# Performance work log

Hardware: AMD Instinct MI355X
Metric: run time of the kernel (lower is better)

## Reference

```python
import jax, jax.numpy as jnp
import numpy as np

IN_FEATURES = 1024
OUT_FEATURES = 1024
GRID_SIZE = 8
SPLINE_ORDER = 3
NUM_CTRL = GRID_SIZE + SPLINE_ORDER  # 11


def _make_grid():
    h = 2.0 / GRID_SIZE
    return jnp.linspace(-1.0 - SPLINE_ORDER * h, 1.0 + SPLINE_ORDER * h,
                        GRID_SIZE + 2 * SPLINE_ORDER + 1, dtype=jnp.float32)  # [15]


def b_splines(t, grid, order):
    # t: [B, F] (already tanh'd). Vectorized over all features at once —
    # the torch per-feature Python loop computes identical math per column.
    te = t[..., None]  # [B, F, 1]
    basis = ((te >= grid[:-1]) & (te < grid[1:])).astype(t.dtype)  # [B, F, G-1]
    for k in range(1, order + 1):
        left_den = grid[k:-1] - grid[:-k - 1]
        left_den = jnp.where(left_den == 0, jnp.ones_like(left_den), left_den)
        left = (te - grid[:-k - 1]) / left_den * basis[..., :-1]
        right_den = grid[k + 1:] - grid[1:-k]
        right_den = jnp.where(right_den == 0, jnp.ones_like(right_den), right_den)
        right = (grid[k + 1:] - te) / right_den * basis[..., 1:]
        basis = left + right
    return basis  # [B, F, NUM_CTRL]


def setup_inputs() -> dict:
    key = jax.random.key(0)
    kx, kc, kw = jax.random.split(key, 3)
    x = jax.random.normal(kx, (4096, IN_FEATURES), dtype=jnp.float32)
    coeffs = jax.random.normal(kc, (IN_FEATURES, OUT_FEATURES, NUM_CTRL), dtype=jnp.float32) * 0.05
    base_weight = jax.random.normal(kw, (IN_FEATURES, OUT_FEATURES), dtype=jnp.float32) * 0.05
    grid = _make_grid()
    return {"x": x, "coeffs": coeffs, "base_weight": base_weight, "grid": grid}


def reference(x, coeffs, base_weight, grid):
    bases = b_splines(jnp.tanh(x), grid, SPLINE_ORDER)          # [B, in, n]
    activation = jnp.einsum('bin,ion->bo', bases, coeffs)        # [B, out]
    residual = x @ base_weight                                   # [B, out]
    return activation + residual
```

## Files before the change

kernel.cpp:

```cpp
#include <hip/hip_runtime.h>
#include <hip/hip_bf16.h>

typedef __attribute__((ext_vector_type(8))) short bf16x8;
typedef __attribute__((ext_vector_type(4))) float f32x4;
typedef __attribute__((ext_vector_type(8))) unsigned short u16x8;

#define M_DIM 4096
#define N_DIM 1024
#define IN_F  1024
#define K_DIM 12288
#define KS4   4
#define KPART (K_DIM / KS4)
#define BK 64
#define NT (KPART / BK)

__device__ __forceinline__ unsigned short f2b(float v) {
  __hip_bfloat16 h = __float2bfloat16(v);
  return *reinterpret_cast<unsigned short*>(&h);
}

__device__ __forceinline__ float fast_tanh(float x) {
  float e = __expf(2.0f * x);
  return 1.0f - 2.0f / (e + 1.0f);
}

__device__ __forceinline__ void spline12(float xv, float* w) {
  float t  = fast_tanh(xv);
  float tf = (t + 1.75f) * 4.0f;
  int j = (int)tf;
  j = j < 3 ? 3 : (j > 10 ? 10 : j);
  float u  = tf - (float)j;
  float um = 1.0f - u;
  float u2 = u * u;
  float w0 = um * um * um * (1.0f / 6.0f);
  float w1 = (0.5f * u - 1.0f) * u2 + (2.0f / 3.0f);
  float w2 = ((-0.5f * u + 0.5f) * u + 0.5f) * u + (1.0f / 6.0f);
  float w3 = u * u2 * (1.0f / 6.0f);
  int base = j - 3;
  #pragma unroll
  for (int s = 0; s < 11; ++s) {
    int r = s - base;
    w[s] = (r == 0) ? w0 : (r == 1) ? w1 : (r == 2) ? w2 : (r == 3) ? w3 : 0.0f;
  }
  w[11] = xv;
}

__global__ __launch_bounds__(256) void bases_kernel(const float* __restrict__ x,
                                                    unsigned short* __restrict__ A) {
  __shared__ unsigned short sb[256 * 24];
  const int tid = threadIdx.x;
  int e0 = blockIdx.x * 512 + tid * 2;
  float2 xv = *(const float2*)(x + e0);
  float w0[12], w1[12];
  spline12(xv.x, w0);
  spline12(xv.y, w1);
  #pragma unroll
  for (int s = 0; s < 12; ++s) { sb[tid * 24 + s] = f2b(w0[s]); sb[tid * 24 + 12 + s] = f2b(w1[s]); }
  __syncthreads();
  u16x8* dst = (u16x8*)(A + (size_t)blockIdx.x * 512 * 12);
  const u16x8* src = (const u16x8*)sb;
  #pragma unroll
  for (int k = 0; k < 3; ++k) dst[tid + k * 256] = src[tid + k * 256];
}

__global__ __launch_bounds__(256) void repack_kernel(const float* __restrict__ coeffs,
                                                     const float* __restrict__ W,
                                                     unsigned short* __restrict__ Bt) {
  __shared__ float lc[64 * 180];
  __shared__ float lw[64 * 20];
  const int o0 = blockIdx.x * 16;
  const int i0 = blockIdx.y * 64;
  const int tid = threadIdx.x;
  #pragma unroll
  for (int it = 0; it < 11; ++it) {
    int v = it * 256 + tid;
    int i = v / 44, c = v - i * 44;
    f32x4 d = *(const f32x4*)(coeffs + ((size_t)(i0 + i) * 1024 + o0) * 11 + c * 4);
    *(f32x4*)(lc + i * 180 + c * 4) = d;
  }
  #pragma unroll
  for (int it = 0; it < 4; ++it) {
    int e = it * 256 + tid;
    int i = e >> 4, ol = e & 15;
    lw[i * 20 + ol] = W[(size_t)(i0 + i) * 1024 + o0 + ol];
  }
  __syncthreads();
  #pragma unroll
  for (int it = 0; it < 6; ++it) {
    int v = it * 256 + tid;
    int ol = v / 96, c = v - ol * 96;
    unsigned short h[8];
    #pragma unroll
    for (int s = 0; s < 8; ++s) {
      int g = c * 8 + s;
      int i = g / 12, n = g - i * 12;
      float val = (n < 11) ? lc[i * 180 + ol * 11 + n] : lw[i * 20 + ol];
      h[s] = f2b(val);
    }
    *(u16x8*)(Bt + (size_t)(o0 + ol) * K_DIM + (size_t)i0 * 12 + c * 8) =
        (u16x8){h[0], h[1], h[2], h[3], h[4], h[5], h[6], h[7]};
  }
}

__device__ __forceinline__ void async16(const void* g, void* l) {
  __builtin_amdgcn_global_load_lds(
      (const __attribute__((address_space(1))) void*)g,
      (__attribute__((address_space(3))) void*)l, 16, 0, 0);
}

__global__ __launch_bounds__(512, 2) void gemm_kernel(const unsigned short* __restrict__ A,
                                                      const unsigned short* __restrict__ Bt,
                                                      float* __restrict__ out) {
  __shared__ __align__(16) unsigned short lds[65536];
  char* lp = (char*)lds;
  const int AS[2] = {0, 32768};
  const int BS[2] = {65536, 98304};

  const int tid  = threadIdx.x;
  const int lane = tid & 63;
  const int wid  = tid >> 6;
  const int wm   = wid >> 2;
  const int wn   = wid & 3;

  const int blk = blockIdx.x;
  const int xcd = blk & 7;
  const int q   = blk >> 3;
  const int bm  = xcd * 2 + (q & 1);
  const int r2  = q >> 1;
  const int bn  = r2 & 3;
  const int ks  = r2 >> 2;
  const size_t m0 = (size_t)bm * 256;
  const size_t n0 = (size_t)bn * 256;
  const size_t ksbyte = (size_t)ks * KPART * 2;

  const char* srcA[4]; const char* srcB[4]; int ldso[4];
  #pragma unroll
  for (int p = 0; p < 4; ++p) {
    int g  = p * 512 + tid;
    int rr = g >> 3, cp = g & 7;
    int cs = cp ^ (rr & 7);
    srcA[p] = (const char*)A  + ((m0 + rr) * (size_t)K_DIM) * 2 + ksbyte + cs * 16;
    srcB[p] = (const char*)Bt + ((n0 + rr) * (size_t)K_DIM) * 2 + ksbyte + cs * 16;
    ldso[p] = g * 16;
  }

  auto stage = [&](int slot, int tile) {
    size_t kb = (size_t)tile * 128;
    #pragma unroll
    for (int p = 0; p < 4; ++p) async16(srcA[p] + kb, lp + AS[slot] + ldso[p]);
    #pragma unroll
    for (int p = 0; p < 4; ++p) async16(srcB[p] + kb, lp + BS[slot] + ldso[p]);
  };

  int offA[8], offB[4];
  #pragma unroll
  for (int m = 0; m < 8; ++m) {
    int row = wm * 128 + m * 16 + (lane & 15);
    int ck  = (lane >> 4) ^ (row & 7);
    offA[m] = row * 128 + ck * 16;
  }
  #pragma unroll
  for (int n = 0; n < 4; ++n) {
    int rowb = wn * 64 + n * 16 + (lane & 15);
    int ckb  = (lane >> 4) ^ (rowb & 7);
    offB[n] = rowb * 128 + ckb * 16;
  }

  f32x4 acc[8][4];
  #pragma unroll
  for (int m = 0; m < 8; ++m)
    #pragma unroll
    for (int n = 0; n < 4; ++n) acc[m][n] = (f32x4){0.f, 0.f, 0.f, 0.f};

  stage(0, 0);
  stage(1, 1);

  for (int t = 0; t < NT; ++t) {
    const int cur = t & 1;
    if (t < NT - 1) asm volatile("s_waitcnt vmcnt(8)" ::: "memory");
    else            asm volatile("s_waitcnt vmcnt(0)" ::: "memory");
    __builtin_amdgcn_s_barrier();
    __builtin_amdgcn_sched_barrier(0);
    asm volatile("" ::: "memory");

    __builtin_amdgcn_s_setprio(1);
    #pragma unroll
    for (int kk = 0; kk < 2; ++kk) {
      const int kx = kk * 64;
      bf16x8 a[8], b[4];
      #pragma unroll
      for (int m = 0; m < 8; ++m) a[m] = *(const bf16x8*)(lp + AS[cur] + (offA[m] ^ kx));
      #pragma unroll
      for (int n = 0; n < 4; ++n) b[n] = *(const bf16x8*)(lp + BS[cur] + (offB[n] ^ kx));
      #pragma unroll
      for (int m = 0; m < 8; ++m)
        #pragma unroll
        for (int n = 0; n < 4; ++n)
          acc[m][n] = __builtin_amdgcn_mfma_f32_16x16x32_bf16(a[m], b[n], acc[m][n], 0, 0, 0);
    }
    __builtin_amdgcn_s_setprio(0);

    asm volatile("" ::: "memory");
    __builtin_amdgcn_sched_barrier(0);
    __builtin_amdgcn_s_barrier();

    if (t + 2 < NT) stage(cur, t + 2);
  }

  const int lr = (lane >> 4) * 4;
  const int lc = lane & 15;
  #pragma unroll
  for (int m = 0; m < 8; ++m)
    #pragma unroll
    for (int n = 0; n < 4; ++n)
      #pragma unroll
      for (int j = 0; j < 4; ++j)
        atomicAdd(&out[(m0 + wm * 128 + m * 16 + lr + j) * N_DIM + n0 + wn * 64 + n * 16 + lc],
                  acc[m][n][j]);
}

__global__ __launch_bounds__(256) void fallback_kernel(const float* __restrict__ x,
                                                       const float* __restrict__ coeffs,
                                                       const float* __restrict__ W,
                                                       float* __restrict__ out) {
  __shared__ float bas[16][64][12];
  const int o0 = blockIdx.x * 64;
  const int b0 = blockIdx.y * 16;
  const int tid = threadIdx.x;
  const int o = tid & 63, bg = tid >> 6;
  float acc[4] = {0.f, 0.f, 0.f, 0.f};
  for (int ic = 0; ic < 16; ++ic) {
    __syncthreads();
    #pragma unroll
    for (int p = 0; p < 4; ++p) {
      int pp = tid + p * 256;
      int bb = pp >> 6, il = pp & 63;
      float w[12];
      spline12(x[(size_t)(b0 + bb) * 1024 + ic * 64 + il], w);
      #pragma unroll
      for (int n = 0; n < 12; ++n) bas[bb][il][n] = w[n];
    }
    __syncthreads();
    for (int il = 0; il < 64; ++il) {
      int gi = ic * 64 + il;
      const float* cp = coeffs + ((size_t)gi * 1024 + o0 + o) * 11;
      float cf[12];
      #pragma unroll
      for (int n = 0; n < 11; ++n) cf[n] = cp[n];
      cf[11] = W[(size_t)gi * 1024 + o0 + o];
      #pragma unroll
      for (int bb = 0; bb < 4; ++bb) {
        float s = 0.f;
        #pragma unroll
        for (int n = 0; n < 12; ++n) s += bas[bg * 4 + bb][il][n] * cf[n];
        acc[bb] += s;
      }
    }
  }
  #pragma unroll
  for (int bb = 0; bb < 4; ++bb)
    out[(size_t)(b0 + bg * 4 + bb) * 1024 + o0 + o] = acc[bb];
}

extern "C" void kernel_launch(void* const* d_in, const int* in_sizes, int n_in,
                              void* d_out, int out_size, void* d_ws, size_t ws_size,
                              hipStream_t stream) {
  const float* x      = (const float*)d_in[0];
  const float* coeffs = (const float*)d_in[1];
  const float* W      = (const float*)d_in[2];
  float* out = (float*)d_out;

  const size_t needA = (size_t)M_DIM * K_DIM * 2;
  const size_t needB = (size_t)N_DIM * K_DIM * 2;

  if (ws_size >= needA + needB) {
    unsigned short* Abuf = (unsigned short*)d_ws;
    unsigned short* Btuf = (unsigned short*)((char*)d_ws + needA);
    hipMemsetAsync(out, 0, (size_t)out_size * sizeof(float), stream);
    bases_kernel<<<dim3(M_DIM * IN_F / 512), dim3(256), 0, stream>>>(x, Abuf);
    repack_kernel<<<dim3(64, 16), dim3(256), 0, stream>>>(coeffs, W, Btuf);
    gemm_kernel<<<dim3(256), dim3(512), 0, stream>>>(Abuf, Btuf, out);
  } else {
    fallback_kernel<<<dim3(16, 256), dim3(256), 0, stream>>>(x, coeffs, W, out);
  }
}
```

Baseline: 263.8 us.

## Retile GEMM to 256x128 blocks with triple-buffered 32-wide K chunks

The GEMM tile changes from 256x256 with 512 threads to 256x128 with 256 threads (4 waves, each still 128x64), so the grid grows from 256 to 512 blocks. The K step shrinks from 64 to 32 per stage and uses a three-slot LDS ring, with a paired-row swizzled layout so a 64-byte row chunk fills one 128-byte LDS line. This cuts LDS per block to about 72KB and deepens prefetch, aiming for better occupancy and latency hiding. The cost is more barriers per unit of K, and reuse drops because B tiles are narrower, so A is fetched twice as often.

```diff
diff --git a/kernel.cpp b/kernel.cpp
--- a/kernel.cpp
+++ b/kernel.cpp
@@ -11,8 +11,7 @@
 #define K_DIM 12288
 #define KS4   4
 #define KPART (K_DIM / KS4)
-#define BK 64
-#define NT (KPART / BK)
+#define NC    (KPART / 32)
 
 __device__ __forceinline__ unsigned short f2b(float v) {
   __hip_bfloat16 h = __float2bfloat16(v);
@@ -108,62 +107,73 @@
       (__attribute__((address_space(3))) void*)l, 16, 0, 0);
 }
 
-__global__ __launch_bounds__(512, 2) void gemm_kernel(const unsigned short* __restrict__ A,
+#define REG_SZ 24576
+#define B_OFF  16384
+
+__global__ __launch_bounds__(256, 2) void gemm_kernel(const unsigned short* __restrict__ A,
                                                       const unsigned short* __restrict__ Bt,
                                                       float* __restrict__ out) {
-  __shared__ __align__(16) unsigned short lds[65536];
+  __shared__ __align__(16) unsigned short lds[36864];
   char* lp = (char*)lds;
-  const int AS[2] = {0, 32768};
-  const int BS[2] = {65536, 98304};
 
   const int tid  = threadIdx.x;
   const int lane = tid & 63;
   const int wid  = tid >> 6;
-  const int wm   = wid >> 2;
-  const int wn   = wid & 3;
+  const int wm   = wid >> 1, wn = wid & 1;
 
   const int blk = blockIdx.x;
   const int xcd = blk & 7;
-  const int q   = blk >> 3;
-  const int bm  = xcd * 2 + (q & 1);
-  const int r2  = q >> 1;
-  const int bn  = r2 & 3;
-  const int ks  = r2 >> 2;
+  const int idx = blk >> 3;
+  const int bm  = xcd * 2 + (idx & 1);
+  const int rst = idx >> 1;
+  const int bn  = rst & 7;
+  const int ks  = rst >> 3;
   const size_t m0 = (size_t)bm * 256;
-  const size_t n0 = (size_t)bn * 256;
+  const size_t n0 = (size_t)bn * 128;
   const size_t ksbyte = (size_t)ks * KPART * 2;
 
-  const char* srcA[4]; const char* srcB[4]; int ldso[4];
-  #pragma unroll
-  for (int p = 0; p < 4; ++p) {
-    int g  = p * 512 + tid;
-    int rr = g >> 3, cp = g & 7;
-    int cs = cp ^ (rr & 7);
-    srcA[p] = (const char*)A  + ((m0 + rr) * (size_t)K_DIM) * 2 + ksbyte + cs * 16;
-    srcB[p] = (const char*)Bt + ((n0 + rr) * (size_t)K_DIM) * 2 + ksbyte + cs * 16;
-    ldso[p] = g * 16;
-  }
-
-  auto stage = [&](int slot, int tile) {
-    size_t kb = (size_t)tile * 128;
-    #pragma unroll
-    for (int p = 0; p < 4; ++p) async16(srcA[p] + kb, lp + AS[slot] + ldso[p]);
-    #pragma unroll
-    for (int p = 0; p < 4; ++p) async16(srcB[p] + kb, lp + BS[slot] + ldso[p]);
+  const char* src[6]; int ldst[6];
+  #pragma unroll
+  for (int q = 0; q < 6; ++q) {
+    if (q < 4) {
+      int g  = q * 256 + tid;
+      int rp = g >> 3, cp = g & 7;
+      int c  = cp ^ (rp & 7);
+      int row = (rp << 1) | (c >> 2);
+      src[q]  = (const char*)A + ((m0 + row) * (size_t)K_DIM) * 2 + ksbyte + (c & 3) * 16;
+      ldst[q] = g * 16;
+    } else {
+      int g  = (q - 4) * 256 + tid;
+      int rp = g >> 3, cp = g & 7;
+      int c  = cp ^ (rp & 7);
+      int row = (rp << 1) | (c >> 2);
+      src[q]  = (const char*)Bt + ((n0 + row) * (size_t)K_DIM) * 2 + ksbyte + (c & 3) * 16;
+      ldst[q] = B_OFF + g * 16;
+    }
+  }
+
+  auto stage = [&](int reg, int chunk) {
+    size_t kb = (size_t)chunk * 64;
+    char* rb = lp + reg * REG_SZ;
+    #pragma unroll
+    for (int q = 0; q < 6; ++q) async16(src[q] + kb, rb + ldst[q]);
   };
 
+  const int c2 = lane >> 4;
   int offA[8], offB[4];
   #pragma unroll
   for (int m = 0; m < 8; ++m) {
-    int row = wm * 128 + m * 16 + (lane & 15);
-    int ck  = (lane >> 4) ^ (row & 7);
-    offA[m] = row * 128 + ck * 16;
+    int r  = wm * 128 + m * 16 + (lane & 15);
+    int rp = r >> 1;
+    int cp = (((r & 1) << 2) | c2) ^ (rp & 7);
+    offA[m] = rp * 128 + cp * 16;
   }
   #pragma unroll
   for (int n = 0; n < 4; ++n) {
-    int rowb = wn * 64 + n * 16 + (lane & 15);
-    int ckb  = (lane >> 4) ^ (rowb & 7);
-    offB[n] = rowb * 128 + ckb * 16;
+    int r  = wn * 64 + n * 16 + (lane & 15);
+    int rp = r >> 1;
+    int cp = (((r & 1) << 2) | c2) ^ (rp & 7);
+    offB[n] = B_OFF + rp * 128 + cp * 16;
   }
 
   f32x4 acc[8][4];
@@ -174,24 +184,25 @@
 
   stage(0, 0);
   stage(1, 1);
-
-  for (int t = 0; t < NT; ++t) {
-    const int cur = t & 1;
-    if (t < NT - 1) asm volatile("s_waitcnt vmcnt(8)" ::: "memory");
-    else            asm volatile("s_waitcnt vmcnt(0)" ::: "memory");
+  stage(2, 2);
+
+  int reg = 0;
+  for (int c = 0; c < NC; ++c) {
+    if (c < NC - 2)       asm volatile("s_waitcnt vmcnt(12)" ::: "memory");
+    else if (c == NC - 2) asm volatile("s_waitcnt vmcnt(6)"  ::: "memory");
+    else                  asm volatile("s_waitcnt vmcnt(0)"  ::: "memory");
     __builtin_amdgcn_s_barrier();
     __builtin_amdgcn_sched_barrier(0);
     asm volatile("" ::: "memory");
 
+    char* rb = lp + reg * REG_SZ;
     __builtin_amdgcn_s_setprio(1);
-    #pragma unroll
-    for (int kk = 0; kk < 2; ++kk) {
-      const int kx = kk * 64;
+    {
       bf16x8 a[8], b[4];
       #pragma unroll
-      for (int m = 0; m < 8; ++m) a[m] = *(const bf16x8*)(lp + AS[cur] + (offA[m] ^ kx));
-      #pragma unroll
-      for (int n = 0; n < 4; ++n) b[n] = *(const bf16x8*)(lp + BS[cur] + (offB[n] ^ kx));
+      for (int m = 0; m < 8; ++m) a[m] = *(const bf16x8*)(rb + offA[m]);
+      #pragma unroll
+      for (int n = 0; n < 4; ++n) b[n] = *(const bf16x8*)(rb + offB[n]);
       #pragma unroll
       for (int m = 0; m < 8; ++m)
         #pragma unroll
@@ -204,7 +215,8 @@
     __builtin_amdgcn_sched_barrier(0);
     __builtin_amdgcn_s_barrier();
 
-    if (t + 2 < NT) stage(cur, t + 2);
+    if (c + 3 < NC) stage(reg, c + 3);
+    reg = (reg == 2) ? 0 : reg + 1;
   }
 
   const int lr = (lane >> 4) * 4;
@@ -279,7 +291,7 @@
     hipMemsetAsync(out, 0, (size_t)out_size * sizeof(float), stream);
     bases_kernel<<<dim3(M_DIM * IN_F / 512), dim3(256), 0, stream>>>(x, Abuf);
     repack_kernel<<<dim3(64, 16), dim3(256), 0, stream>>>(coeffs, W, Btuf);
-    gemm_kernel<<<dim3(256), dim3(512), 0, stream>>>(Abuf, Btuf, out);
+    gemm_kernel<<<dim3(512), dim3(256), 0, stream>>>(Abuf, Btuf, out);
   } else {
     fallback_kernel<<<dim3(16, 256), dim3(256), 0, stream>>>(x, coeffs, W, out);
   }
```

Result: no change. 265.0 us (+0.5%).
